# Performance work log

Hardware: AMD Instinct MI355X
Metric: run time of the kernel (lower is better)

## Reference

```python
import jax, jax.numpy as jnp
import numpy as np

EMBED_DIM = 768
NUM_HEADS = 12
HEAD_DIM = EMBED_DIM // NUM_HEADS


def setup_inputs() -> dict:
    key = jax.random.key(0)
    k1, k2, k3, k4 = jax.random.split(key, 4)
    B, N, D = 8, 1024, EMBED_DIM
    x = jax.random.normal(k1, (B, N, D), dtype=jnp.float32)
    # qkv Linear (no bias): torch weight [3D, D]; we store transposed [D, 3D]
    W_qkv = jax.random.normal(k2, (D, 3 * D), dtype=jnp.float32) * (D ** -0.5)
    # projection Linear with bias
    W_proj = jax.random.normal(k3, (D, D), dtype=jnp.float32) * (D ** -0.5)
    b_proj = jax.random.normal(k4, (D,), dtype=jnp.float32) * 0.01
    return {"x": x, "W_qkv": W_qkv, "W_proj": W_proj, "b_proj": b_proj}


def reference(x, W_qkv, W_proj, b_proj):
    B, N, D = x.shape
    h, d = NUM_HEADS, HEAD_DIM
    scaling = d ** -0.5
    qkv = x @ W_qkv  # [B, N, 3D]
    # 'b n (qkv h d) -> qkv b h n d'
    qkv = qkv.reshape(B, N, 3, h, d).transpose(2, 0, 3, 1, 4)
    q, k, v = qkv[0], qkv[1], qkv[2]  # each [B, h, N, d]
    energy = jnp.einsum('bhid,bhjd->bhij', q, k) * scaling  # [B, h, N, N]
    att = jax.nn.softmax(energy, axis=-1)
    out = jnp.einsum('bhij,bhjd->bhid', att, v)  # [B, h, N, d]
    out = out.transpose(0, 2, 1, 3).reshape(B, N, D)  # 'b h n d -> b n (h d)'
    out = out @ W_proj + b_proj
    return out
```

## Files before the change

### kernel.cpp

```cpp
#include <hip/hip_runtime.h>
#include <hip/hip_bf16.h>

#define NUM_B 8
#define SEQ   1024
#define DIM   768
#define NH    12
#define HD    64

typedef __bf16 bf16x8 __attribute__((ext_vector_type(8)));
typedef float  f32x4  __attribute__((ext_vector_type(4)));
typedef unsigned int u32;

#define QSCL 0.18033688011112042f

__device__ __forceinline__ unsigned short f2bf(float f) {
  unsigned int u = __float_as_uint(f);
  u += 0x7FFFu + ((u >> 16) & 1u);
  return (unsigned short)(u >> 16);
}

__device__ __forceinline__ float fexp2(float x) { return __builtin_exp2f(x); }

__device__ __forceinline__ u32 pk2bf(float a, float b) {
  return (u32)f2bf(a) | ((u32)f2bf(b) << 16);
}

__device__ __forceinline__ void gload_lds16(const void* g, void* l) {
  __builtin_amdgcn_global_load_lds(
      (const __attribute__((address_space(1))) unsigned int*)g,
      (__attribute__((address_space(3))) unsigned int*)l, 16, 0, 0);
}

__global__ void cvt_kernel(const float* __restrict__ in, unsigned short* __restrict__ out, int n) {
  int i = (blockIdx.x * blockDim.x + threadIdx.x) * 4;
  if (i >= n) return;
  float4 v = *(const float4*)(in + i);
  ushort4 o = { f2bf(v.x), f2bf(v.y), f2bf(v.z), f2bf(v.w) };
  *(ushort4*)(out + i) = o;
}

__global__ void tcvt_kernel(const float* __restrict__ in, unsigned short* __restrict__ out,
                            int R, int C) {
  __shared__ unsigned short tile[32][33];
  int c0 = blockIdx.x * 32, r0 = blockIdx.y * 32;
  int tx = threadIdx.x, ty = threadIdx.y;
  #pragma unroll
  for (int i = 0; i < 32; i += 8)
    tile[ty + i][tx] = f2bf(in[(size_t)(r0 + ty + i) * C + c0 + tx]);
  __syncthreads();
  #pragma unroll
  for (int i = 0; i < 32; i += 8)
    out[(size_t)(c0 + ty + i) * R + r0 + tx] = tile[tx][ty + i];
}

template<bool QKV>
__global__ __launch_bounds__(256) void gemm_bf16(
    const unsigned short* __restrict__ A,
    const unsigned short* __restrict__ Bt,
    int K,
    unsigned short* __restrict__ qb,
    unsigned short* __restrict__ kb,
    unsigned short* __restrict__ vt,
    float* __restrict__ outp,
    const float* __restrict__ bias)
{
  __shared__ short As[128][40];
  __shared__ short Bs[128][40];
  const int m0 = blockIdx.x * 128, n0 = blockIdx.y * 128;
  const int t = threadIdx.x;
  const int lane = t & 63, w = t >> 6;
  const int l15 = lane & 15, g = lane >> 4;
  const int wm = w >> 1, wn = w & 1;
  const int ar = t >> 2, ac = (t & 3) * 8;

  f32x4 zv = {0.f, 0.f, 0.f, 0.f};
  f32x4 acc[4][4];
  #pragma unroll
  for (int i = 0; i < 4; ++i)
    #pragma unroll
    for (int j = 0; j < 4; ++j) acc[i][j] = zv;

  const size_t szK = (size_t)K;
  for (int k0 = 0; k0 < K; k0 += 32) {
    int4 a0 = *(const int4*)(A  + (size_t)(m0 + ar)      * szK + k0 + ac);
    int4 a1 = *(const int4*)(A  + (size_t)(m0 + ar + 64) * szK + k0 + ac);
    int4 b0 = *(const int4*)(Bt + (size_t)(n0 + ar)      * szK + k0 + ac);
    int4 b1 = *(const int4*)(Bt + (size_t)(n0 + ar + 64) * szK + k0 + ac);
    __syncthreads();
    *(int4*)&As[ar][ac]      = a0;
    *(int4*)&As[ar + 64][ac] = a1;
    *(int4*)&Bs[ar][ac]      = b0;
    *(int4*)&Bs[ar + 64][ac] = b1;
    __syncthreads();
    bf16x8 af[4], bfr[4];
    #pragma unroll
    for (int i = 0; i < 4; ++i) af[i]  = *(const bf16x8*)&As[wm*64 + i*16 + l15][g*8];
    #pragma unroll
    for (int i = 0; i < 4; ++i) bfr[i] = *(const bf16x8*)&Bs[wn*64 + i*16 + l15][g*8];
    #pragma unroll
    for (int i = 0; i < 4; ++i)
      #pragma unroll
      for (int j = 0; j < 4; ++j)
        acc[i][j] = __builtin_amdgcn_mfma_f32_16x16x32_bf16(af[i], bfr[j], acc[i][j], 0, 0, 0);
  }

  const int mbase = m0 + wm * 64, nbase = n0 + wn * 64;
  if (QKV) {
    #pragma unroll
    for (int i = 0; i < 4; ++i) {
      #pragma unroll
      for (int j = 0; j < 4; ++j) {
        int n = nbase + j * 16 + l15;
        int which = n / DIM;
        int jr = n - which * DIM;
        int head = jr >> 6, dd = jr & 63;
        float sc = (which == 0) ? QSCL : 1.0f;
        #pragma unroll
        for (int r = 0; r < 4; ++r) {
          int m = mbase + i * 16 + g * 4 + r;
          int bb = m >> 10, nn = m & 1023;
          unsigned short val = f2bf(acc[i][j][r] * sc);
          size_t bh = (size_t)bb * NH + head;
          if (which == 0)      qb[(bh * SEQ + nn) * HD + dd] = val;
          else if (which == 1) kb[(bh * SEQ + nn) * HD + dd] = val;
          else {
            int nnp = (nn & ~31) | ((nn & 12) << 1) | ((nn & 16) >> 2) | (nn & 3);
            vt[(bh * HD + dd) * SEQ + nnp] = val;
          }
        }
      }
    }
  } else {
    #pragma unroll
    for (int i = 0; i < 4; ++i)
      #pragma unroll
      for (int j = 0; j < 4; ++j) {
        int n = nbase + j * 16 + l15;
        float bv = bias[n];
        #pragma unroll
        for (int r = 0; r < 4; ++r) {
          int m = mbase + i * 16 + g * 4 + r;
          outp[(size_t)m * DIM + n] = acc[i][j][r] + bv;
        }
      }
  }
}

__global__ __launch_bounds__(256) void attn_kernel(
    const unsigned short* __restrict__ qb,
    const unsigned short* __restrict__ kb,
    const unsigned short* __restrict__ vt,
    unsigned short* __restrict__ ao)
{
  __shared__ short lds[2][2][4096];
  const int bid = blockIdx.x;
  const int qt = (bid & 7) * 128;
  const int bh = bid >> 3;
  const int t = threadIdx.x, lane = t & 63, w = t >> 6;
  const int l15 = lane & 15, g = lane >> 4;
  const unsigned short* Qp = qb + (size_t)bh * SEQ * HD;
  const unsigned short* Kp = kb + (size_t)bh * SEQ * HD;
  const unsigned short* Vp = vt + (size_t)bh * HD * SEQ;
  const int q0 = qt + w * 32;
  const int swz = l15 & 7;

  int offK[2], offV[2], ldso[2];
  #pragma unroll
  for (int i = 0; i < 2; ++i) {
    int chunk = ((w * 2 + i) << 6) + lane;
    int row = chunk >> 3;
    int c = (chunk & 7) ^ (row & 7);
    offK[i] = row * HD + c * 8;
    offV[i] = row * SEQ + c * 8;
    ldso[i] = (w * 2 + i) << 9;
  }

  bf16x8 bq[2][2];
  #pragma unroll
  for (int nq = 0; nq < 2; ++nq)
    #pragma unroll
    for (int kk = 0; kk < 2; ++kk)
      bq[nq][kk] = *(const bf16x8*)(Qp + (size_t)(q0 + nq*16 + l15) * HD + kk*32 + g*8);

  f32x4 zv = {0.f, 0.f, 0.f, 0.f};
  f32x4 accO[2][4];
  float m_[2] = { -INFINITY, -INFINITY };
  float l_[2] = { 0.f, 0.f };
  #pragma unroll
  for (int nq = 0; nq < 2; ++nq)
    #pragma unroll
    for (int fn = 0; fn < 4; ++fn) accO[nq][fn] = zv;

  #pragma unroll
  for (int i = 0; i < 2; ++i) {
    gload_lds16(Kp + offK[i], &lds[0][0][ldso[i]]);
    gload_lds16(Vp + offV[i], &lds[0][1][ldso[i]]);
  }
  asm volatile("s_waitcnt vmcnt(0)" ::: "memory");
  __syncthreads();

  int cur = 0;
  for (int kt = 0; kt < SEQ; kt += 64) {
    if (kt + 64 < SEQ) {
      #pragma unroll
      for (int i = 0; i < 2; ++i) {
        gload_lds16(Kp + (size_t)(kt + 64) * HD + offK[i], &lds[cur ^ 1][0][ldso[i]]);
        gload_lds16(Vp + (kt + 64) + offV[i], &lds[cur ^ 1][1][ldso[i]]);
      }
    }
    const short* Kb = &lds[cur][0][0];
    const short* Vb = &lds[cur][1][0];

    f32x4 s[2][4];
    #pragma unroll
    for (int nq = 0; nq < 2; ++nq)
      #pragma unroll
      for (int fm = 0; fm < 4; ++fm) s[nq][fm] = zv;
    #pragma unroll
    for (int fm = 0; fm < 4; ++fm)
      #pragma unroll
      for (int kk = 0; kk < 2; ++kk) {
        bf16x8 ak = *(const bf16x8*)&Kb[(fm*16 + l15) * 64 + (((kk*4 + g) ^ swz) << 3)];
        s[0][fm] = __builtin_amdgcn_mfma_f32_16x16x32_bf16(ak, bq[0][kk], s[0][fm], 0, 0, 0);
        s[1][fm] = __builtin_amdgcn_mfma_f32_16x16x32_bf16(ak, bq[1][kk], s[1][fm], 0, 0, 0);
      }

    bf16x8 av[4][2];
    #pragma unroll
    for (int fn = 0; fn < 4; ++fn)
      #pragma unroll
      for (int cc = 0; cc < 2; ++cc)
        av[fn][cc] = *(const bf16x8*)&Vb[(fn*16 + l15) * 64 + (((cc*4 + g) ^ swz) << 3)];

    u32 bp[2][2][4];
    #pragma unroll
    for (int nq = 0; nq < 2; ++nq) {
      f32x4 mc;
      #pragma unroll
      for (int r = 0; r < 4; ++r)
        mc[r] = fmaxf(fmaxf(s[nq][0][r], s[nq][1][r]), fmaxf(s[nq][2][r], s[nq][3][r]));
      float mx = fmaxf(fmaxf(mc[0], mc[1]), fmaxf(mc[2], mc[3]));
      mx = fmaxf(mx, __shfl_xor(mx, 16, 64));
      mx = fmaxf(mx, __shfl_xor(mx, 32, 64));
      float mo = m_[nq];
      if (__any(mx > mo + 11.0f)) {
        float mn = fmaxf(mo, mx);
        float al = fexp2(mo - mn);
        m_[nq] = mn;
        l_[nq] *= al;
        #pragma unroll
        for (int fn = 0; fn < 4; ++fn)
          #pragma unroll
          for (int r = 0; r < 4; ++r) accO[nq][fn][r] *= al;
      }
      float mn = m_[nq];
      float p[4][4];
      #pragma unroll
      for (int fm = 0; fm < 4; ++fm)
        #pragma unroll
        for (int r = 0; r < 4; ++r)
          p[fm][r] = fexp2(s[nq][fm][r] - mn);
      float rs = ((p[0][0] + p[0][1]) + (p[0][2] + p[0][3]))
               + ((p[1][0] + p[1][1]) + (p[1][2] + p[1][3]))
               + ((p[2][0] + p[2][1]) + (p[2][2] + p[2][3]))
               + ((p[3][0] + p[3][1]) + (p[3][2] + p[3][3]));
      rs += __shfl_xor(rs, 16, 64);
      rs += __shfl_xor(rs, 32, 64);
      l_[nq] += rs;
      #pragma unroll
      for (int fm = 0; fm < 4; ++fm) {
        int cc = fm >> 1, wi = (fm & 1) * 2;
        bp[nq][cc][wi]     = pk2bf(p[fm][0], p[fm][1]);
        bp[nq][cc][wi + 1] = pk2bf(p[fm][2], p[fm][3]);
      }
    }

    #pragma unroll
    for (int cc = 0; cc < 2; ++cc) {
      union { u32 u[4]; bf16x8 v; } b0, b1;
      #pragma unroll
      for (int i = 0; i < 4; ++i) { b0.u[i] = bp[0][cc][i]; b1.u[i] = bp[1][cc][i]; }
      #pragma unroll
      for (int fn = 0; fn < 4; ++fn) {
        accO[0][fn] = __builtin_amdgcn_mfma_f32_16x16x32_bf16(av[fn][cc], b0.v, accO[0][fn], 0, 0, 0);
        accO[1][fn] = __builtin_amdgcn_mfma_f32_16x16x32_bf16(av[fn][cc], b1.v, accO[1][fn], 0, 0, 0);
      }
    }

    asm volatile("s_waitcnt vmcnt(0)" ::: "memory");
    __syncthreads();
    cur ^= 1;
  }

  const int bb = bh / NH, hh = bh - bb * NH;
  #pragma unroll
  for (int nq = 0; nq < 2; ++nq) {
    float inv = 1.0f / l_[nq];
    int q = q0 + nq * 16 + l15;
    unsigned short* op = ao + ((size_t)(bb * SEQ + q)) * DIM + hh * HD + g * 4;
    #pragma unroll
    for (int fn = 0; fn < 4; ++fn) {
      ushort4 o = { f2bf(accO[nq][fn][0] * inv), f2bf(accO[nq][fn][1] * inv),
                    f2bf(accO[nq][fn][2] * inv), f2bf(accO[nq][fn][3] * inv) };
      *(ushort4*)(op + fn * 16) = o;
    }
  }
}

extern "C" void kernel_launch(void* const* d_in, const int* in_sizes, int n_in,
                              void* d_out, int out_size, void* d_ws, size_t ws_size,
                              hipStream_t stream) {
  const float* x     = (const float*)d_in[0];
  const float* Wqkv  = (const float*)d_in[1];
  const float* Wproj = (const float*)d_in[2];
  const float* bproj = (const float*)d_in[3];
  float* out = (float*)d_out;

  unsigned short* ws = (unsigned short*)d_ws;
  const size_t NX = (size_t)NUM_B * SEQ * DIM;
  unsigned short* x_bf    = ws;
  unsigned short* Wqkv_t  = x_bf + NX;
  unsigned short* Wproj_t = Wqkv_t + (size_t)3 * DIM * DIM;
  unsigned short* qbuf    = Wproj_t + (size_t)DIM * DIM;
  unsigned short* kbuf    = qbuf + NX;
  unsigned short* vtb     = kbuf + NX;
  unsigned short* attb    = vtb + NX;

  cvt_kernel<<<dim3((unsigned)(NX / 4 / 256)), 256, 0, stream>>>(x, x_bf, (int)NX);
  tcvt_kernel<<<dim3(3 * DIM / 32, DIM / 32), dim3(32, 8), 0, stream>>>(Wqkv, Wqkv_t, DIM, 3 * DIM);
  tcvt_kernel<<<dim3(DIM / 32, DIM / 32), dim3(32, 8), 0, stream>>>(Wproj, Wproj_t, DIM, DIM);

  gemm_bf16<true><<<dim3(64, 18), 256, 0, stream>>>(
      x_bf, Wqkv_t, DIM, qbuf, kbuf, vtb, nullptr, nullptr);

  attn_kernel<<<dim3(NUM_B * NH * (SEQ / 128)), 256, 0, stream>>>(qbuf, kbuf, vtb, attb);

  gemm_bf16<false><<<dim3(64, 6), 256, 0, stream>>>(
      attb, Wproj_t, DIM, nullptr, nullptr, nullptr, out, bproj);
}
```

Before: 233.0 us.

## Use direct-to-LDS loads in GEMM and MFMA row sums in attention

The GEMM now stages its A and B tiles with global_load_lds directly into unpadded shared memory instead of going through registers, which removes the register round-trip and the explicit LDS stores. The attention kernel computes the softmax row sums with an MFMA against a ones vector on the bf16-rounded probabilities, replacing the scalar adds and cross-lane shuffles. It also converts probabilities with the native bf16 cast instead of the manual rounding routine. In exchange, the GEMM loses its LDS padding and may see bank conflicts, it waits on the loads each iteration with no overlap, and the row sum is now taken from bf16 values rather than fp32.

```diff
diff --git a/kernel.cpp b/kernel.cpp
--- a/kernel.cpp
+++ b/kernel.cpp
@@ -20,10 +20,6 @@
 }
 
 __device__ __forceinline__ float fexp2(float x) { return __builtin_exp2f(x); }
-
-__device__ __forceinline__ u32 pk2bf(float a, float b) {
-  return (u32)f2bf(a) | ((u32)f2bf(b) << 16);
-}
 
 __device__ __forceinline__ void gload_lds16(const void* g, void* l) {
   __builtin_amdgcn_global_load_lds(
@@ -64,14 +60,24 @@
     float* __restrict__ outp,
     const float* __restrict__ bias)
 {
-  __shared__ short As[128][40];
-  __shared__ short Bs[128][40];
+  __shared__ short As[128 * 32];
+  __shared__ short Bs[128 * 32];
   const int m0 = blockIdx.x * 128, n0 = blockIdx.y * 128;
   const int t = threadIdx.x;
   const int lane = t & 63, w = t >> 6;
   const int l15 = lane & 15, g = lane >> 4;
   const int wm = w >> 1, wn = w & 1;
-  const int ar = t >> 2, ac = (t & 3) * 8;
+
+  const int ch0 = t, ch1 = t + 256;
+  const size_t szK = (size_t)K;
+  const unsigned short* Ag0 = A  + (size_t)(m0 + (ch0 >> 2)) * szK + (ch0 & 3) * 8;
+  const unsigned short* Ag1 = A  + (size_t)(m0 + (ch1 >> 2)) * szK + (ch1 & 3) * 8;
+  const unsigned short* Bg0 = Bt + (size_t)(n0 + (ch0 >> 2)) * szK + (ch0 & 3) * 8;
+  const unsigned short* Bg1 = Bt + (size_t)(n0 + (ch1 >> 2)) * szK + (ch1 & 3) * 8;
+  short* Al0 = &As[w * 512];
+  short* Al1 = Al0 + 2048;
+  short* Bl0 = &Bs[w * 512];
+  short* Bl1 = Bl0 + 2048;
 
   f32x4 zv = {0.f, 0.f, 0.f, 0.f};
   f32x4 acc[4][4];
@@ -80,23 +86,19 @@
     #pragma unroll
     for (int j = 0; j < 4; ++j) acc[i][j] = zv;
 
-  const size_t szK = (size_t)K;
   for (int k0 = 0; k0 < K; k0 += 32) {
-    int4 a0 = *(const int4*)(A  + (size_t)(m0 + ar)      * szK + k0 + ac);
-    int4 a1 = *(const int4*)(A  + (size_t)(m0 + ar + 64) * szK + k0 + ac);
-    int4 b0 = *(const int4*)(Bt + (size_t)(n0 + ar)      * szK + k0 + ac);
-    int4 b1 = *(const int4*)(Bt + (size_t)(n0 + ar + 64) * szK + k0 + ac);
     __syncthreads();
-    *(int4*)&As[ar][ac]      = a0;
-    *(int4*)&As[ar + 64][ac] = a1;
-    *(int4*)&Bs[ar][ac]      = b0;
-    *(int4*)&Bs[ar + 64][ac] = b1;
+    gload_lds16(Ag0 + k0, Al0);
+    gload_lds16(Ag1 + k0, Al1);
+    gload_lds16(Bg0 + k0, Bl0);
+    gload_lds16(Bg1 + k0, Bl1);
+    asm volatile("s_waitcnt vmcnt(0)" ::: "memory");
     __syncthreads();
     bf16x8 af[4], bfr[4];
     #pragma unroll
-    for (int i = 0; i < 4; ++i) af[i]  = *(const bf16x8*)&As[wm*64 + i*16 + l15][g*8];
-    #pragma unroll
-    for (int i = 0; i < 4; ++i) bfr[i] = *(const bf16x8*)&Bs[wn*64 + i*16 + l15][g*8];
+    for (int i = 0; i < 4; ++i) af[i]  = *(const bf16x8*)&As[(wm*64 + i*16 + l15) * 32 + g*8];
+    #pragma unroll
+    for (int i = 0; i < 4; ++i) bfr[i] = *(const bf16x8*)&Bs[(wn*64 + i*16 + l15) * 32 + g*8];
     #pragma unroll
     for (int i = 0; i < 4; ++i)
       #pragma unroll
@@ -182,10 +184,14 @@
     for (int kk = 0; kk < 2; ++kk)
       bq[nq][kk] = *(const bf16x8*)(Qp + (size_t)(q0 + nq*16 + l15) * HD + kk*32 + g*8);
 
+  bf16x8 ones;
+  #pragma unroll
+  for (int i = 0; i < 8; ++i) ones[i] = (__bf16)1.0f;
+
   f32x4 zv = {0.f, 0.f, 0.f, 0.f};
   f32x4 accO[2][4];
+  f32x4 rsac[2] = { zv, zv };
   float m_[2] = { -INFINITY, -INFINITY };
-  float l_[2] = { 0.f, 0.f };
   #pragma unroll
   for (int nq = 0; nq < 2; ++nq)
     #pragma unroll
@@ -232,7 +238,7 @@
       for (int cc = 0; cc < 2; ++cc)
         av[fn][cc] = *(const bf16x8*)&Vb[(fn*16 + l15) * 64 + (((cc*4 + g) ^ swz) << 3)];
 
-    u32 bp[2][2][4];
+    bf16x8 pb[2][2];
     #pragma unroll
     for (int nq = 0; nq < 2; ++nq) {
       f32x4 mc;
@@ -247,45 +253,31 @@
         float mn = fmaxf(mo, mx);
         float al = fexp2(mo - mn);
         m_[nq] = mn;
-        l_[nq] *= al;
+        rsac[nq] *= al;
         #pragma unroll
         for (int fn = 0; fn < 4; ++fn)
           #pragma unroll
           for (int r = 0; r < 4; ++r) accO[nq][fn][r] *= al;
       }
       float mn = m_[nq];
-      float p[4][4];
-      #pragma unroll
-      for (int fm = 0; fm < 4; ++fm)
+      #pragma unroll
+      for (int cc = 0; cc < 2; ++cc)
         #pragma unroll
-        for (int r = 0; r < 4; ++r)
-          p[fm][r] = fexp2(s[nq][fm][r] - mn);
-      float rs = ((p[0][0] + p[0][1]) + (p[0][2] + p[0][3]))
-               + ((p[1][0] + p[1][1]) + (p[1][2] + p[1][3]))
-               + ((p[2][0] + p[2][1]) + (p[2][2] + p[2][3]))
-               + ((p[3][0] + p[3][1]) + (p[3][2] + p[3][3]));
-      rs += __shfl_xor(rs, 16, 64);
-      rs += __shfl_xor(rs, 32, 64);
-      l_[nq] += rs;
-      #pragma unroll
-      for (int fm = 0; fm < 4; ++fm) {
-        int cc = fm >> 1, wi = (fm & 1) * 2;
-        bp[nq][cc][wi]     = pk2bf(p[fm][0], p[fm][1]);
-        bp[nq][cc][wi + 1] = pk2bf(p[fm][2], p[fm][3]);
-      }
+        for (int h = 0; h < 2; ++h)
+          #pragma unroll
+          for (int r = 0; r < 4; ++r)
+            pb[nq][cc][h*4 + r] = (__bf16)fexp2(s[nq][2*cc + h][r] - mn);
+      rsac[nq] = __builtin_amdgcn_mfma_f32_16x16x32_bf16(ones, pb[nq][0], rsac[nq], 0, 0, 0);
+      rsac[nq] = __builtin_amdgcn_mfma_f32_16x16x32_bf16(ones, pb[nq][1], rsac[nq], 0, 0, 0);
     }
 
     #pragma unroll
-    for (int cc = 0; cc < 2; ++cc) {
-      union { u32 u[4]; bf16x8 v; } b0, b1;
-      #pragma unroll
-      for (int i = 0; i < 4; ++i) { b0.u[i] = bp[0][cc][i]; b1.u[i] = bp[1][cc][i]; }
+    for (int cc = 0; cc < 2; ++cc)
       #pragma unroll
       for (int fn = 0; fn < 4; ++fn) {
-        accO[0][fn] = __builtin_amdgcn_mfma_f32_16x16x32_bf16(av[fn][cc], b0.v, accO[0][fn], 0, 0, 0);
-        accO[1][fn] = __builtin_amdgcn_mfma_f32_16x16x32_bf16(av[fn][cc], b1.v, accO[1][fn], 0, 0, 0);
-      }
-    }
+        accO[0][fn] = __builtin_amdgcn_mfma_f32_16x16x32_bf16(av[fn][cc], pb[0][cc], accO[0][fn], 0, 0, 0);
+        accO[1][fn] = __builtin_amdgcn_mfma_f32_16x16x32_bf16(av[fn][cc], pb[1][cc], accO[1][fn], 0, 0, 0);
+      }
 
     asm volatile("s_waitcnt vmcnt(0)" ::: "memory");
     __syncthreads();
@@ -295,7 +287,7 @@
   const int bb = bh / NH, hh = bh - bb * NH;
   #pragma unroll
   for (int nq = 0; nq < 2; ++nq) {
-    float inv = 1.0f / l_[nq];
+    float inv = 1.0f / rsac[nq][0];
     int q = q0 + nq * 16 + l15;
     unsigned short* op = ao + ((size_t)(bb * SEQ + q)) * DIM + hh * HD + g * 4;
     #pragma unroll
```

Result: faster. 224.0 us (-3.9%).
